# Kernel optimization log

Hardware: AMD Instinct MI355X
Metric: run time of the kernel (lower is better)

The kernel has to match this reference:

```python
import jax, jax.numpy as jnp
import numpy as np

B, N, D, H, MLP = 8, 1024, 1024, 16, 4096
DEPTH = D // H
EPS = 1e-6
INV_SQRT_DEPTH = 1.0 / np.sqrt(DEPTH).astype(np.float32)


def _linear_params(key, fan_in, fan_out):
    w = jax.random.normal(key, (fan_in, fan_out), dtype=jnp.float32) * 0.02
    b = jnp.zeros((fan_out,), dtype=jnp.float32)
    return w, b


def setup_inputs() -> dict:
    key = jax.random.key(0)
    ks = jax.random.split(key, 20)
    inp = {}
    inp['inputs'] = jax.random.normal(ks[0], (B, N, D), dtype=jnp.float32)
    inp['z'] = jax.random.normal(ks[1], (B, D), dtype=jnp.float32)
    # norm1 conditioning MLPs
    inp['n1_hw'], inp['n1_hb'] = _linear_params(ks[2], D, D)
    inp['n1_gw'], inp['n1_gb'] = _linear_params(ks[3], D, D)
    inp['n1_bw'], inp['n1_bb'] = _linear_params(ks[4], D, D)
    # attention
    inp['wq_w'], inp['wq_b'] = _linear_params(ks[5], D, D)
    inp['wk_w'], inp['wk_b'] = _linear_params(ks[6], D, D)
    inp['wv_w'], inp['wv_b'] = _linear_params(ks[7], D, D)
    inp['qa_w'], inp['qa_b'] = _linear_params(ks[8], D, H)
    inp['out_w'], inp['out_b'] = _linear_params(ks[9], D, D)
    # norm2 conditioning MLPs
    inp['n2_hw'], inp['n2_hb'] = _linear_params(ks[10], D, D)
    inp['n2_gw'], inp['n2_gb'] = _linear_params(ks[11], D, D)
    inp['n2_bw'], inp['n2_bb'] = _linear_params(ks[12], D, D)
    # MLP
    inp['mlp_w1'], inp['mlp_b1'] = _linear_params(ks[13], D, MLP)
    inp['mlp_w2'], inp['mlp_b2'] = _linear_params(ks[14], MLP, D)
    return inp


def _sm_norm(x, z, hw, hb, gw, gb, bw, bb):
    # LayerNorm over last dim, no affine
    mean = jnp.mean(x, axis=-1, keepdims=True)
    var = jnp.mean(jnp.square(x - mean), axis=-1, keepdims=True)
    xn = (x - mean) / jnp.sqrt(var + EPS)
    h = jax.nn.relu(z @ hw + hb)                 # [B, D]
    scale = (h @ gw + gb)[:, :, None]            # [B, D, 1]
    shift = (h @ bw + bb)[:, :, None]            # [B, D, 1]
    # broadcasts since N == D (as in the torch module)
    return xn * scale + shift


def _additive_attn(x, wq_w, wq_b, wk_w, wk_b, wv_w, wv_b, qa_w, qa_b, out_w, out_b):
    q = x @ wq_w + wq_b                          # [B, N, D]
    k = x @ wk_w + wk_b
    v = x @ wv_w + wv_b
    attn = jnp.transpose(q @ qa_w + qa_b, (0, 2, 1)) * INV_SQRT_DEPTH  # [B, H, N]
    attn = jax.nn.softmax(attn, axis=-1)
    qh = q.reshape(B, N, H, DEPTH).transpose(0, 2, 1, 3)  # [B, H, N, d]
    kh = k.reshape(B, N, H, DEPTH).transpose(0, 2, 1, 3)
    vh = v.reshape(B, N, H, DEPTH).transpose(0, 2, 1, 3)
    global_q = jnp.einsum('bhn,bhnd->bhd', attn, qh)[:, :, None, :]  # [B, H, 1, d]
    r = global_q * kh * vh                       # [B, H, N, d]
    r = r.transpose(0, 2, 1, 3).reshape(B, N, D)
    return r @ out_w + out_b, attn


def reference(inputs, z,
              n1_hw, n1_hb, n1_gw, n1_gb, n1_bw, n1_bb,
              wq_w, wq_b, wk_w, wk_b, wv_w, wv_b, qa_w, qa_b, out_w, out_b,
              n2_hw, n2_hb, n2_gw, n2_gb, n2_bw, n2_bb,
              mlp_w1, mlp_b1, mlp_w2, mlp_b2):
    x_norm1 = _sm_norm(inputs, z, n1_hw, n1_hb, n1_gw, n1_gb, n1_bw, n1_bb)
    attn_out, attn_maps = _additive_attn(x_norm1, wq_w, wq_b, wk_w, wk_b,
                                         wv_w, wv_b, qa_w, qa_b, out_w, out_b)
    attn_out = inputs + attn_out                 # dropout rate 0 -> identity
    x_norm2 = _sm_norm(attn_out, z, n2_hw, n2_hb, n2_gw, n2_gb, n2_bw, n2_bb)
    h = jax.nn.gelu(x_norm2 @ mlp_w1 + mlp_b1, approximate=False)
    mlp_out = h @ mlp_w2 + mlp_b2
    output = attn_out + mlp_out
    return output, attn_maps
```

## Files before the change

### kernel.cpp

```cpp
#include <hip/hip_runtime.h>
#include <math.h>


typedef __attribute__((ext_vector_type(8))) short short8;
typedef __attribute__((ext_vector_type(4))) float f32x4;

#define DEVI __device__ __forceinline__

DEVI unsigned short f2bf(float f) {
  union { float f; unsigned int u; } c; c.f = f;
  unsigned int r = c.u + 0x7fffu + ((c.u >> 16) & 1u);
  return (unsigned short)(r >> 16);
}
DEVI float bf2f(unsigned short u) {
  union { unsigned int u; float f; } c; c.u = ((unsigned int)u) << 16;
  return c.f;
}

DEVI void async16(const void* g, void* l) {
  __builtin_amdgcn_global_load_lds((const __attribute__((address_space(1))) void*)g,
                                   (__attribute__((address_space(3))) void*)l, 16, 0, 0);
}

__global__ void transpose_bf16_k(const float* __restrict__ in,
                                 unsigned short* __restrict__ out, int R, int C) {
  __shared__ float tile[32][33];
  const int c0 = blockIdx.x * 32, r0 = blockIdx.y * 32;
  const int tx = threadIdx.x, ty = threadIdx.y;
#pragma unroll
  for (int j = 0; j < 4; j++) {
    int r = r0 + ty + j * 8, c = c0 + tx;
    if (r < R && c < C) tile[ty + j * 8][tx] = in[(size_t)r * C + c];
  }
  __syncthreads();
#pragma unroll
  for (int j = 0; j < 4; j++) {
    int c = c0 + ty + j * 8, r = r0 + tx;
    if (c < C && r < R) out[(size_t)c * R + r] = f2bf(tile[tx][ty + j * 8]);
  }
}

__global__ void pad_bias_k(const float* __restrict__ qa_b, float* __restrict__ pad) {
  int t = threadIdx.x;
  pad[t] = (t < 16) ? qa_b[t] : 0.f;
}

__global__ void bias3_k(const float* __restrict__ b0, const float* __restrict__ b1,
                        const float* __restrict__ b2, float* __restrict__ out) {
  const int t = blockIdx.x * 256 + threadIdx.x;
  out[t] = (t < 1024) ? b0[t] : (t < 2048 ? b1[t - 1024] : b2[t - 2048]);
}

__global__ void zero_k(float4* __restrict__ p) {
  p[blockIdx.x * 256 + threadIdx.x] = float4{0.f, 0.f, 0.f, 0.f};
}

template <int NMAT>
__global__ __launch_bounds__(256) void skinny_k(const float* __restrict__ X,
                                                const float* __restrict__ W0,
                                                const float* __restrict__ W1,
                                                float* __restrict__ acc0,
                                                float* __restrict__ acc1) {
  const int tid = threadIdx.x;
  const int jt = blockIdx.x, kc = blockIdx.y;
  const int jl = tid & 63, kg = tid >> 6;
  const int jcol = jt * 64 + jl;
  __shared__ float xs[8][64];
  for (int i = tid; i < 512; i += 256) {
    const int b = i >> 6, kk = i & 63;
    xs[b][kk] = X[b * 1024 + kc * 64 + kk];
  }
  __syncthreads();
  float a0[8], a1[8];
#pragma unroll
  for (int b = 0; b < 8; b++) { a0[b] = 0.f; a1[b] = 0.f; }
#pragma unroll
  for (int kk = 0; kk < 16; kk++) {
    const int k = kg * 16 + kk;
    const float w0 = W0[(size_t)(kc * 64 + k) * 1024 + jcol];
#pragma unroll
    for (int b = 0; b < 8; b++) a0[b] += xs[b][k] * w0;
    if (NMAT == 2) {
      const float w1 = W1[(size_t)(kc * 64 + k) * 1024 + jcol];
#pragma unroll
      for (int b = 0; b < 8; b++) a1[b] += xs[b][k] * w1;
    }
  }
  __shared__ float red[256][9];
#pragma unroll
  for (int b = 0; b < 8; b++) red[tid][b] = a0[b];
  __syncthreads();
  if (tid < 64) {
#pragma unroll
    for (int b = 0; b < 8; b++) {
      const float s = red[tid][b] + red[tid + 64][b] + red[tid + 128][b] + red[tid + 192][b];
      atomicAdd(&acc0[b * 1024 + jcol], s);
    }
  }
  if (NMAT == 2) {
    __syncthreads();
#pragma unroll
    for (int b = 0; b < 8; b++) red[tid][b] = a1[b];
    __syncthreads();
    if (tid < 64) {
#pragma unroll
      for (int b = 0; b < 8; b++) {
        const float s = red[tid][b] + red[tid + 64][b] + red[tid + 128][b] + red[tid + 192][b];
        atomicAdd(&acc1[b * 1024 + jcol], s);
      }
    }
  }
}

__global__ void h_epi_k(const float* __restrict__ acc, const float* __restrict__ hb,
                        float* __restrict__ h) {
  const int i = blockIdx.x * 256 + threadIdx.x;
  h[i] = fmaxf(acc[i] + hb[i & 1023], 0.f);
}

__global__ __launch_bounds__(256) void ln_mod_k(const float* __restrict__ x,
                                                const float* __restrict__ s_acc,
                                                const float* __restrict__ t_acc,
                                                const float* __restrict__ gb,
                                                const float* __restrict__ bb,
                                                unsigned short* __restrict__ out) {
  const int lane = threadIdx.x & 63, wid = threadIdx.x >> 6;
  const size_t row = (size_t)blockIdx.x * 4 + wid;
  const int n = (int)(row & 1023);
  const float4* xr = (const float4*)(x + row * 1024);
  float4 v[4];
  float s = 0.f, ss = 0.f;
#pragma unroll
  for (int j = 0; j < 4; j++) {
    v[j] = xr[j * 64 + lane];
    s += v[j].x + v[j].y + v[j].z + v[j].w;
    ss += v[j].x * v[j].x + v[j].y * v[j].y + v[j].z * v[j].z + v[j].w * v[j].w;
  }
#pragma unroll
  for (int o = 32; o > 0; o >>= 1) { s += __shfl_xor(s, o); ss += __shfl_xor(ss, o); }
  const float mean = s * (1.f / 1024.f);
  const float var = ss * (1.f / 1024.f) - mean * mean;
  const float inv = rsqrtf(var + 1e-6f);
  const float scale = s_acc[row] + gb[n];
  const float shift = t_acc[row] + bb[n];
  const float sc = scale * inv;
  const float sh = shift - mean * sc;
#pragma unroll
  for (int j = 0; j < 4; j++) {
    ushort4 o4;
    o4.x = f2bf(v[j].x * sc + sh);
    o4.y = f2bf(v[j].y * sc + sh);
    o4.z = f2bf(v[j].z * sc + sh);
    o4.w = f2bf(v[j].w * sc + sh);
    *(ushort4*)(out + row * 1024 + (size_t)(j * 64 + lane) * 4) = o4;
  }
}

template <int EPI, int BM>
__global__ __launch_bounds__(512, 2) void gemm256(const unsigned short* __restrict__ A,
                                                  const unsigned short* __restrict__ BT,
                                                  const float* __restrict__ bias,
                                                  const float* __restrict__ resid,
                                                  void* __restrict__ Cout,
                                                  int M, int N, int K) {
  constexpr bool SWAP = (EPI == 0 || EPI == 1);
  constexpr int WROWS = BM / 2;
  constexpr int MF = WROWS / 16;
  constexpr int ALOADS = (BM * 8) / 512;
  constexpr int NLOADS = ALOADS + 4;
  __shared__ unsigned short lds[2 * BM * 64 + 2 * 256 * 64];
  unsigned short* As0 = lds;
  unsigned short* Bs0 = lds + 2 * BM * 64;
  const int tid = threadIdx.x;
  const int lane = tid & 63, w = tid >> 6;
  const int wm = w >> 2, wn = w & 3;
  const int lr = lane & 15;
  const int g0 = lane >> 4;
  const int nwg = gridDim.x * gridDim.y;
  const int rb = blockIdx.y * gridDim.x + blockIdx.x;
  const int sb = (rb & 7) * (nwg >> 3) + (rb >> 3);
  const size_t brow = (size_t)(sb / gridDim.x) * BM;
  const size_t bcol = (size_t)(sb % gridDim.x) * 256;
  const unsigned short* Ab = A + brow * (size_t)K;
  const unsigned short* Bb = BT + bcol * (size_t)K;
  const int NT = K >> 6;

  const f32x4 zero = {0.f, 0.f, 0.f, 0.f};
  f32x4 acc[MF][4];
#pragma unroll
  for (int m = 0; m < MF; m++)
#pragma unroll
    for (int n = 0; n < 4; n++) acc[m][n] = zero;

  auto stage = [&](int k0, int d) {
#pragma unroll
    for (int i = 0; i < ALOADS; i++) {
      const int c = i * 512 + tid;
      const int r = c >> 3, g = c & 7;
      const int gl = g ^ (r & 7);
      async16(Ab + (size_t)r * K + (k0 + gl * 8), &As0[(size_t)d * BM * 64 + c * 8]);
    }
#pragma unroll
    for (int i = 0; i < 4; i++) {
      const int c = i * 512 + tid;
      const int r = c >> 3, g = c & 7;
      const int gl = g ^ (r & 7);
      async16(Bb + (size_t)r * K + (k0 + gl * 8), &Bs0[(size_t)d * 256 * 64 + c * 8]);
    }
  };

  stage(0, 0);
  stage(64, 1);
  if constexpr (NLOADS == 8) asm volatile("s_waitcnt vmcnt(8)" ::: "memory");
  else asm volatile("s_waitcnt vmcnt(6)" ::: "memory");
  __builtin_amdgcn_s_barrier();

  for (int t = 0; t < NT; ++t) {
    const unsigned short* as = As0 + (size_t)(t & 1) * BM * 64;
    const unsigned short* bs = Bs0 + (size_t)(t & 1) * 256 * 64;
#pragma unroll
    for (int kk = 0; kk < 64; kk += 32) {
      const int gk = (kk >> 3) + g0;
      short8 bfrag[4];
#pragma unroll
      for (int nf = 0; nf < 4; nf++) {
        const int r = wn * 64 + nf * 16 + lr;
        bfrag[nf] = *(const short8*)&bs[r * 64 + ((gk ^ (r & 7)) << 3)];
      }
      __builtin_amdgcn_s_setprio(1);
#pragma unroll
      for (int mf = 0; mf < MF; mf++) {
        const int r = wm * WROWS + mf * 16 + lr;
        const short8 afrag = *(const short8*)&as[r * 64 + ((gk ^ (r & 7)) << 3)];
#pragma unroll
        for (int nf = 0; nf < 4; nf++) {
          if constexpr (SWAP)
            acc[mf][nf] = __builtin_amdgcn_mfma_f32_16x16x32_bf16(bfrag[nf], afrag, acc[mf][nf], 0, 0, 0);
          else
            acc[mf][nf] = __builtin_amdgcn_mfma_f32_16x16x32_bf16(afrag, bfrag[nf], acc[mf][nf], 0, 0, 0);
        }
      }
      __builtin_amdgcn_s_setprio(0);
    }
    asm volatile("" ::: "memory");
    __builtin_amdgcn_s_barrier();
    if (t + 2 < NT) {
      stage((t + 2) << 6, t & 1);
      if constexpr (NLOADS == 8) asm volatile("s_waitcnt vmcnt(8)" ::: "memory");
      else asm volatile("s_waitcnt vmcnt(6)" ::: "memory");
    } else {
      asm volatile("s_waitcnt vmcnt(0)" ::: "memory");
    }
    __builtin_amdgcn_s_barrier();
  }

  if constexpr (SWAP) {
    unsigned short* cst = lds;
    const int g4 = (lane >> 4) * 4;
#pragma unroll
    for (int nf = 0; nf < 4; nf++) {
#pragma unroll
      for (int mf = 0; mf < MF; mf++) {
        const int row = wm * WROWS + mf * 16 + lr;
        const int colb = wn * 64 + nf * 16 + g4;
        const float4 bv = *(const float4*)&bias[bcol + colb];
        float v[4];
#pragma unroll
        for (int j = 0; j < 4; j++) {
          v[j] = acc[mf][nf][j] + (&bv.x)[j];
          if (EPI == 1) v[j] = 0.5f * v[j] * (1.0f + erff(v[j] * 0.70710678118654752f));
        }
        ushort4 p;
        p.x = f2bf(v[0]); p.y = f2bf(v[1]); p.z = f2bf(v[2]); p.w = f2bf(v[3]);
        const int byo = row * 512 + ((colb * 2) ^ ((row & 7) << 4));
        *(ushort4*)((char*)cst + byo) = p;
      }
    }
    __syncthreads();
    unsigned short* outp;
    size_t ostride;
    if (EPI == 0) {
      outp = (unsigned short*)Cout + (size_t)(bcol >> 10) * ((size_t)M << 10) + (bcol & 1023);
      ostride = 1024;
    } else {
      outp = (unsigned short*)Cout + bcol;
      ostride = (size_t)N;
    }
#pragma unroll
    for (int it = 0; it < BM / 16; it++) {
      const int fl = it * 4096 + tid * 8;
      const int row = fl >> 8, colu = fl & 255;
      const int byo = row * 512 + ((colu * 2) ^ ((row & 7) << 4));
      const short8 val = *(const short8*)((char*)cst + byo);
      *(short8*)(outp + (size_t)(brow + row) * ostride + colu) = val;
    }
  } else {
    const int lc = lane & 15, lrow = (lane >> 4) * 4;
#pragma unroll
    for (int nf = 0; nf < 4; nf++) {
      const size_t col = bcol + wn * 64 + nf * 16 + lc;
      const float bv = bias[col];
#pragma unroll
      for (int mf = 0; mf < MF; mf++) {
#pragma unroll
        for (int j = 0; j < 4; j++) {
          const size_t row = brow + wm * WROWS + mf * 16 + lrow + j;
          const size_t idx = row * (size_t)N + col;
          ((float*)Cout)[idx] = acc[mf][nf][j] + bv + resid[idx];
        }
      }
    }
  }
}

template <int EPI>
__global__ __launch_bounds__(256) void gemm_bf16(const unsigned short* __restrict__ A,
                                                 const unsigned short* __restrict__ BT,
                                                 const float* __restrict__ bias,
                                                 const float* __restrict__ resid,
                                                 void* __restrict__ Cout,
                                                 int M, int N, int K) {
  __shared__ unsigned short As[128 * 64];
  __shared__ unsigned short Bs[128 * 64];
  const int tid = threadIdx.x;
  const int lane = tid & 63, wid = tid >> 6;
  const int wr = wid >> 1, wc = wid & 1;
  const size_t brow = (size_t)blockIdx.y * 128;
  const size_t bcol = (size_t)blockIdx.x * 128;
  const unsigned short* Ab = A + brow * (size_t)K;
  const unsigned short* Bb = BT + bcol * (size_t)K;

  const f32x4 zero = {0.f, 0.f, 0.f, 0.f};
  f32x4 acc[4][4];
#pragma unroll
  for (int m = 0; m < 4; m++)
#pragma unroll
    for (int n = 0; n < 4; n++) acc[m][n] = zero;

  for (int k0 = 0; k0 < K; k0 += 64) {
#pragma unroll
    for (int i = 0; i < 4; i++) {
      const int eo = (i * 256 + tid) * 8;
      const int r = eo >> 6, c = eo & 63;
      async16(Ab + (size_t)r * K + (k0 + c), &As[eo]);
      async16(Bb + (size_t)r * K + (k0 + c), &Bs[eo]);
    }
    __syncthreads();
    const int lr = lane & 15, lk = (lane >> 4) * 8;
#pragma unroll
    for (int kk = 0; kk < 64; kk += 32) {
      short8 af[4], bfv[4];
#pragma unroll
      for (int m = 0; m < 4; m++)
        af[m] = *(const short8*)&As[(wr * 64 + m * 16 + lr) * 64 + kk + lk];
#pragma unroll
      for (int n = 0; n < 4; n++)
        bfv[n] = *(const short8*)&Bs[(wc * 64 + n * 16 + lr) * 64 + kk + lk];
#pragma unroll
      for (int m = 0; m < 4; m++)
#pragma unroll
        for (int n = 0; n < 4; n++)
          acc[m][n] = __builtin_amdgcn_mfma_f32_16x16x32_bf16(af[m], bfv[n], acc[m][n], 0, 0, 0);
    }
    __syncthreads();
  }

  const int lc = lane & 15, lr4 = (lane >> 4) * 4;
#pragma unroll
  for (int n = 0; n < 4; n++) {
    const size_t col = bcol + wc * 64 + n * 16 + lc;
    const float bv = bias[col];
#pragma unroll
    for (int m = 0; m < 4; m++) {
#pragma unroll
      for (int j = 0; j < 4; j++) {
        const size_t row = brow + wr * 64 + m * 16 + lr4 + j;
        const size_t idx = row * (size_t)N + col;
        ((float*)Cout)[idx] = acc[m][n][j] + bv;
      }
    }
  }
}

__global__ __launch_bounds__(256) void softmax_k(const float* __restrict__ logits,
                                                 float* __restrict__ attn) {
  const int tid = threadIdx.x;
  const int bh = blockIdx.x;
  const int b = bh >> 4, h = bh & 15;
  __shared__ float redm[4];
  __shared__ float reds[4];
  float vals[4];
#pragma unroll
  for (int j = 0; j < 4; j++) {
    const int n = j * 256 + tid;
    vals[j] = logits[((size_t)b * 1024 + n) * 128 + h] * 0.125f;
  }
  float m = fmaxf(fmaxf(vals[0], vals[1]), fmaxf(vals[2], vals[3]));
#pragma unroll
  for (int o = 32; o > 0; o >>= 1) m = fmaxf(m, __shfl_xor(m, o));
  if ((tid & 63) == 0) redm[tid >> 6] = m;
  __syncthreads();
  m = fmaxf(fmaxf(redm[0], redm[1]), fmaxf(redm[2], redm[3]));
  float e[4];
  float s = 0.f;
#pragma unroll
  for (int j = 0; j < 4; j++) { e[j] = expf(vals[j] - m); s += e[j]; }
#pragma unroll
  for (int o = 32; o > 0; o >>= 1) s += __shfl_xor(s, o);
  if ((tid & 63) == 0) reds[tid >> 6] = s;
  __syncthreads();
  s = reds[0] + reds[1] + reds[2] + reds[3];
  const float invs = 1.f / s;
#pragma unroll
  for (int j = 0; j < 4; j++)
    attn[(size_t)bh * 1024 + j * 256 + tid] = e[j] * invs;
}

__global__ __launch_bounds__(256) void global_q_k(const float* __restrict__ attn,
                                                  const unsigned short* __restrict__ Q,
                                                  float* __restrict__ gq) {
  const int tid = threadIdx.x;
  const int bh = blockIdx.x;
  const int b = bh >> 4, h = bh & 15;
  const int d = tid & 63, g = tid >> 6;
  const float* arow = attn + (size_t)bh * 1024;
  const unsigned short* qcol = Q + (size_t)b * 1024 * 1024 + h * 64 + d;
  float acc = 0.f;
  for (int n = g * 256; n < g * 256 + 256; n++)
    acc += arow[n] * bf2f(qcol[(size_t)n * 1024]);
  __shared__ float red[256];
  red[tid] = acc;
  __syncthreads();
  if (g == 0) gq[(size_t)bh * 64 + d] = red[d] + red[64 + d] + red[128 + d] + red[192 + d];
}

__global__ __launch_bounds__(256) void r_k(const unsigned short* __restrict__ Kb,
                                           const unsigned short* __restrict__ Vb,
                                           const float* __restrict__ gq,
                                           unsigned short* __restrict__ R) {
  const size_t i = ((size_t)blockIdx.x * 256 + threadIdx.x) * 8;
  const int col = (int)(i & 1023);
  const size_t b = i >> 20;
  const int h = col >> 6, dd = col & 63;
  const float* g = gq + ((b << 4) + h) * 64 + dd;
  short8 kv = *(const short8*)(Kb + i);
  short8 vv = *(const short8*)(Vb + i);
  short8 r;
#pragma unroll
  for (int j = 0; j < 8; j++) {
    float f = g[j] * bf2f((unsigned short)kv[j]) * bf2f((unsigned short)vv[j]);
    r[j] = (short)f2bf(f);
  }
  *(short8*)(R + i) = r;
}

extern "C" void kernel_launch(void* const* d_in, const int* in_sizes, int n_in,
                              void* d_out, int out_size, void* d_ws, size_t ws_size,
                              hipStream_t stream) {
  (void)in_sizes; (void)n_in; (void)out_size; (void)ws_size;
  const float* inputs = (const float*)d_in[0];
  const float* z      = (const float*)d_in[1];
  const float* n1_hw = (const float*)d_in[2];  const float* n1_hb = (const float*)d_in[3];
  const float* n1_gw = (const float*)d_in[4];  const float* n1_gb = (const float*)d_in[5];
  const float* n1_bw = (const float*)d_in[6];  const float* n1_bb = (const float*)d_in[7];
  const float* wq_w  = (const float*)d_in[8];  const float* wq_b  = (const float*)d_in[9];
  const float* wk_w  = (const float*)d_in[10]; const float* wk_b  = (const float*)d_in[11];
  const float* wv_w  = (const float*)d_in[12]; const float* wv_b  = (const float*)d_in[13];
  const float* qa_w  = (const float*)d_in[14]; const float* qa_b  = (const float*)d_in[15];
  const float* out_w = (const float*)d_in[16]; const float* out_b = (const float*)d_in[17];
  const float* n2_hw = (const float*)d_in[18]; const float* n2_hb = (const float*)d_in[19];
  const float* n2_gw = (const float*)d_in[20]; const float* n2_gb = (const float*)d_in[21];
  const float* n2_bw = (const float*)d_in[22]; const float* n2_bb = (const float*)d_in[23];
  const float* mlp_w1 = (const float*)d_in[24]; const float* mlp_b1 = (const float*)d_in[25];
  const float* mlp_w2 = (const float*)d_in[26]; const float* mlp_b2 = (const float*)d_in[27];

  const int M = 8192, D = 1024, MLPD = 4096;

  char* ws = (char*)d_ws;
  size_t o = 0;
  auto alloc = [&](size_t bytes) -> char* {
    char* p = ws + o;
    o += (bytes + 255) & ~(size_t)255;
    return p;
  };
  unsigned short* wqkvT = (unsigned short*)alloc((size_t)3 * D * D * 2);
  unsigned short* woT = (unsigned short*)alloc((size_t)D * D * 2);
  unsigned short* w1T = (unsigned short*)alloc((size_t)MLPD * D * 2);
  unsigned short* w2T = (unsigned short*)alloc((size_t)D * MLPD * 2);
  unsigned short* qaT = (unsigned short*)alloc((size_t)128 * D * 2);
  unsigned short* xn  = (unsigned short*)alloc((size_t)M * D * 2);
  char* big = alloc((size_t)M * MLPD * 2);
  unsigned short* Qb = (unsigned short*)big;
  unsigned short* Kb = (unsigned short*)(big + (size_t)M * D * 2);
  unsigned short* Vb = (unsigned short*)(big + (size_t)M * D * 4);
  float* logits      = (float*)(big + (size_t)M * D * 6);
  unsigned short* hbuf = (unsigned short*)big;
  float* cacc  = (float*)alloc(6 * 8192 * 4);
  float* accH1 = cacc;
  float* accS1 = cacc + 1 * 8192;
  float* accT1 = cacc + 2 * 8192;
  float* accH2 = cacc + 3 * 8192;
  float* accS2 = cacc + 4 * 8192;
  float* accT2 = cacc + 5 * 8192;
  float* h1     = (float*)alloc(8 * 1024 * 4);
  float* h2     = (float*)alloc(8 * 1024 * 4);
  float* gq     = (float*)alloc(8 * 16 * 64 * 4);
  float* qa_b_pad = (float*)alloc(128 * 4);
  float* qkvb    = (float*)alloc(3072 * 4);

  float* out0 = (float*)d_out;
  float* attn = (float*)d_out + (size_t)M * D;

  const dim3 tb(32, 8);
  hipLaunchKernelGGL(transpose_bf16_k, dim3(32, 32), tb, 0, stream, wq_w, wqkvT, D, D);
  hipLaunchKernelGGL(transpose_bf16_k, dim3(32, 32), tb, 0, stream, wk_w, wqkvT + (size_t)D * D, D, D);
  hipLaunchKernelGGL(transpose_bf16_k, dim3(32, 32), tb, 0, stream, wv_w, wqkvT + (size_t)2 * D * D, D, D);
  hipLaunchKernelGGL(transpose_bf16_k, dim3(32, 32), tb, 0, stream, out_w, woT, D, D);
  hipLaunchKernelGGL(transpose_bf16_k, dim3(128, 32), tb, 0, stream, mlp_w1, w1T, D, MLPD);
  hipLaunchKernelGGL(transpose_bf16_k, dim3(32, 128), tb, 0, stream, mlp_w2, w2T, MLPD, D);
  hipLaunchKernelGGL(transpose_bf16_k, dim3(1, 32), tb, 0, stream, qa_w, qaT, D, 16);
  hipLaunchKernelGGL(pad_bias_k, dim3(1), dim3(128), 0, stream, qa_b, qa_b_pad);
  hipLaunchKernelGGL(bias3_k, dim3(12), dim3(256), 0, stream, wq_b, wk_b, wv_b, qkvb);

  hipLaunchKernelGGL(zero_k, dim3(48), dim3(256), 0, stream, (float4*)cacc);
  hipLaunchKernelGGL(skinny_k<1>, dim3(16, 16), dim3(256), 0, stream, z, n1_hw, (const float*)nullptr, accH1, (float*)nullptr);
  hipLaunchKernelGGL(h_epi_k, dim3(32), dim3(256), 0, stream, accH1, n1_hb, h1);
  hipLaunchKernelGGL(skinny_k<2>, dim3(16, 16), dim3(256), 0, stream, h1, n1_gw, n1_bw, accS1, accT1);
  hipLaunchKernelGGL(skinny_k<1>, dim3(16, 16), dim3(256), 0, stream, z, n2_hw, (const float*)nullptr, accH2, (float*)nullptr);
  hipLaunchKernelGGL(h_epi_k, dim3(32), dim3(256), 0, stream, accH2, n2_hb, h2);
  hipLaunchKernelGGL(skinny_k<2>, dim3(16, 16), dim3(256), 0, stream, h2, n2_gw, n2_bw, accS2, accT2);

  hipLaunchKernelGGL(ln_mod_k, dim3(M / 4), dim3(256), 0, stream, inputs, accS1, accT1, n1_gb, n1_bb, xn);

  hipLaunchKernelGGL((gemm256<0, 256>), dim3(12, 32), dim3(512), 0, stream, xn, wqkvT, qkvb, (const float*)nullptr, (void*)Qb, M, 3072, D);

  hipLaunchKernelGGL(gemm_bf16<3>, dim3(1, 64), dim3(256), 0, stream, Qb, qaT, qa_b_pad, (const float*)nullptr, (void*)logits, M, 128, D);

  hipLaunchKernelGGL(softmax_k, dim3(128), dim3(256), 0, stream, logits, attn);

  hipLaunchKernelGGL(global_q_k, dim3(128), dim3(256), 0, stream, attn, Qb, gq);

  hipLaunchKernelGGL(r_k, dim3(M * D / 8 / 256), dim3(256), 0, stream, Kb, Vb, gq, Kb);

  hipLaunchKernelGGL((gemm256<2, 128>), dim3(4, 64), dim3(512), 0, stream, Kb, woT, out_b, inputs, (void*)out0, M, D, D);

  hipLaunchKernelGGL(ln_mod_k, dim3(M / 4), dim3(256), 0, stream, out0, accS2, accT2, n2_gb, n2_bb, xn);

  hipLaunchKernelGGL((gemm256<1, 256>), dim3(16, 32), dim3(512), 0, stream, xn, w1T, mlp_b1, (const float*)nullptr, (void*)hbuf, M, MLPD, D);

  hipLaunchKernelGGL((gemm256<2, 128>), dim3(4, 64), dim3(512), 0, stream, hbuf, w2T, mlp_b2, out0, (void*)out0, M, D, MLPD);
}
```

Baseline: 667.7 us.

## Split GEMM K-tile into four phases interleaving async loads with MFMA sub-blocks

The bf16 GEMM main loop now divides each 64-wide K tile into four phases, each covering one quarter of the accumulator tile. Each phase issues one quarter of the next tile's global-to-LDS async loads, so memory traffic is spread across the compute instead of being issued in one burst after a barrier. The grouped block-index swizzle is replaced with a direct blockIdx mapping. The trade-off is a barrier after every phase instead of two per tile, and possibly worse L2 reuse now that the swizzle is gone.

Measured after the change: 647.4 us. 1.03x faster.

```diff
diff --git a/kernel.cpp b/kernel.cpp
--- a/kernel.cpp
+++ b/kernel.cpp
@@ -166,8 +166,8 @@
   constexpr bool SWAP = (EPI == 0 || EPI == 1);
   constexpr int WROWS = BM / 2;
   constexpr int MF = WROWS / 16;
-  constexpr int ALOADS = (BM * 8) / 512;
-  constexpr int NLOADS = ALOADS + 4;
+  constexpr int MPH = MF / 2;
+  constexpr int ALOADS_H = (WROWS * 64) / (512 * 8);
   __shared__ unsigned short lds[2 * BM * 64 + 2 * 256 * 64];
   unsigned short* As0 = lds;
   unsigned short* Bs0 = lds + 2 * BM * 64;
@@ -176,11 +176,8 @@
   const int wm = w >> 2, wn = w & 3;
   const int lr = lane & 15;
   const int g0 = lane >> 4;
-  const int nwg = gridDim.x * gridDim.y;
-  const int rb = blockIdx.y * gridDim.x + blockIdx.x;
-  const int sb = (rb & 7) * (nwg >> 3) + (rb >> 3);
-  const size_t brow = (size_t)(sb / gridDim.x) * BM;
-  const size_t bcol = (size_t)(sb % gridDim.x) * 256;
+  const size_t brow = (size_t)blockIdx.y * BM;
+  const size_t bcol = (size_t)blockIdx.x * 256;
   const unsigned short* Ab = A + brow * (size_t)K;
   const unsigned short* Bb = BT + bcol * (size_t)K;
   const int NT = K >> 6;
@@ -192,66 +189,85 @@
 #pragma unroll
     for (int n = 0; n < 4; n++) acc[m][n] = zero;
 
-  auto stage = [&](int k0, int d) {
-#pragma unroll
-    for (int i = 0; i < ALOADS; i++) {
+  auto stageA = [&](int t, int h) {
+    const int d = t & 1, k0 = t << 6;
+#pragma unroll
+    for (int i = 0; i < ALOADS_H; i++) {
       const int c = i * 512 + tid;
-      const int r = c >> 3, g = c & 7;
+      const int r = h * WROWS + (c >> 3), g = c & 7;
       const int gl = g ^ (r & 7);
-      async16(Ab + (size_t)r * K + (k0 + gl * 8), &As0[(size_t)d * BM * 64 + c * 8]);
-    }
-#pragma unroll
-    for (int i = 0; i < 4; i++) {
+      async16(Ab + (size_t)r * K + (k0 + gl * 8),
+              &As0[(size_t)d * BM * 64 + (size_t)h * WROWS * 64 + c * 8]);
+    }
+  };
+  auto stageB = [&](int t, int h) {
+    const int d = t & 1, k0 = t << 6;
+#pragma unroll
+    for (int i = 0; i < 2; i++) {
       const int c = i * 512 + tid;
-      const int r = c >> 3, g = c & 7;
+      const int r = h * 128 + (c >> 3), g = c & 7;
       const int gl = g ^ (r & 7);
-      async16(Bb + (size_t)r * K + (k0 + gl * 8), &Bs0[(size_t)d * 256 * 64 + c * 8]);
+      async16(Bb + (size_t)r * K + (k0 + gl * 8),
+              &Bs0[(size_t)d * 256 * 64 + (size_t)h * 128 * 64 + c * 8]);
     }
   };
 
-  stage(0, 0);
-  stage(64, 1);
-  if constexpr (NLOADS == 8) asm volatile("s_waitcnt vmcnt(8)" ::: "memory");
-  else asm volatile("s_waitcnt vmcnt(6)" ::: "memory");
-  __builtin_amdgcn_s_barrier();
+  stageA(0, 0); stageA(0, 1); stageB(0, 0); stageB(0, 1);
 
   for (int t = 0; t < NT; ++t) {
     const unsigned short* as = As0 + (size_t)(t & 1) * BM * 64;
     const unsigned short* bs = Bs0 + (size_t)(t & 1) * 256 * 64;
 #pragma unroll
-    for (int kk = 0; kk < 64; kk += 32) {
-      const int gk = (kk >> 3) + g0;
-      short8 bfrag[4];
-#pragma unroll
-      for (int nf = 0; nf < 4; nf++) {
-        const int r = wn * 64 + nf * 16 + lr;
-        bfrag[nf] = *(const short8*)&bs[r * 64 + ((gk ^ (r & 7)) << 3)];
+    for (int p = 0; p < 4; ++p) {
+      if (t + 1 < NT) {
+        if (p == 0) stageA(t + 1, 0);
+        else if (p == 1) stageA(t + 1, 1);
+        else if (p == 2) stageB(t + 1, 0);
+        else stageB(t + 1, 1);
+      }
+      if (p == 0) {
+        if (t + 1 < NT) {
+          if constexpr (ALOADS_H == 2) asm volatile("s_waitcnt vmcnt(2)" ::: "memory");
+          else asm volatile("s_waitcnt vmcnt(1)" ::: "memory");
+        } else {
+          asm volatile("s_waitcnt vmcnt(0)" ::: "memory");
+        }
+        __builtin_amdgcn_s_barrier();
+      }
+      const int mf0 = (p >> 1) * MPH;
+      const int nf0 = (p & 1) * 2;
+      short8 bfrag[2][2], afrag[2][MPH];
+#pragma unroll
+      for (int kki = 0; kki < 2; kki++) {
+        const int gk = kki * 4 + g0;
+#pragma unroll
+        for (int nf = 0; nf < 2; nf++) {
+          const int r = wn * 64 + (nf0 + nf) * 16 + lr;
+          bfrag[kki][nf] = *(const short8*)&bs[r * 64 + ((gk ^ (r & 7)) << 3)];
+        }
+#pragma unroll
+        for (int mf = 0; mf < MPH; mf++) {
+          const int r = wm * WROWS + (mf0 + mf) * 16 + lr;
+          afrag[kki][mf] = *(const short8*)&as[r * 64 + ((gk ^ (r & 7)) << 3)];
+        }
       }
       __builtin_amdgcn_s_setprio(1);
 #pragma unroll
-      for (int mf = 0; mf < MF; mf++) {
-        const int r = wm * WROWS + mf * 16 + lr;
-        const short8 afrag = *(const short8*)&as[r * 64 + ((gk ^ (r & 7)) << 3)];
-#pragma unroll
-        for (int nf = 0; nf < 4; nf++) {
-          if constexpr (SWAP)
-            acc[mf][nf] = __builtin_amdgcn_mfma_f32_16x16x32_bf16(bfrag[nf], afrag, acc[mf][nf], 0, 0, 0);
-          else
-            acc[mf][nf] = __builtin_amdgcn_mfma_f32_16x16x32_bf16(afrag, bfrag[nf], acc[mf][nf], 0, 0, 0);
-        }
-      }
+      for (int kki = 0; kki < 2; kki++)
+#pragma unroll
+        for (int mf = 0; mf < MPH; mf++)
+#pragma unroll
+          for (int nf = 0; nf < 2; nf++) {
+            if constexpr (SWAP)
+              acc[mf0 + mf][nf0 + nf] = __builtin_amdgcn_mfma_f32_16x16x32_bf16(
+                  bfrag[kki][nf], afrag[kki][mf], acc[mf0 + mf][nf0 + nf], 0, 0, 0);
+            else
+              acc[mf0 + mf][nf0 + nf] = __builtin_amdgcn_mfma_f32_16x16x32_bf16(
+                  afrag[kki][mf], bfrag[kki][nf], acc[mf0 + mf][nf0 + nf], 0, 0, 0);
+          }
       __builtin_amdgcn_s_setprio(0);
-    }
-    asm volatile("" ::: "memory");
-    __builtin_amdgcn_s_barrier();
-    if (t + 2 < NT) {
-      stage((t + 2) << 6, t & 1);
-      if constexpr (NLOADS == 8) asm volatile("s_waitcnt vmcnt(8)" ::: "memory");
-      else asm volatile("s_waitcnt vmcnt(6)" ::: "memory");
-    } else {
-      asm volatile("s_waitcnt vmcnt(0)" ::: "memory");
-    }
-    __builtin_amdgcn_s_barrier();
+      __builtin_amdgcn_s_barrier();
+    }
   }
 
   if constexpr (SWAP) {
@@ -270,10 +286,10 @@
           v[j] = acc[mf][nf][j] + (&bv.x)[j];
           if (EPI == 1) v[j] = 0.5f * v[j] * (1.0f + erff(v[j] * 0.70710678118654752f));
         }
-        ushort4 p;
-        p.x = f2bf(v[0]); p.y = f2bf(v[1]); p.z = f2bf(v[2]); p.w = f2bf(v[3]);
+        ushort4 pck;
+        pck.x = f2bf(v[0]); pck.y = f2bf(v[1]); pck.z = f2bf(v[2]); pck.w = f2bf(v[3]);
         const int byo = row * 512 + ((colb * 2) ^ ((row & 7) << 4));
-        *(ushort4*)((char*)cst + byo) = p;
+        *(ushort4*)((char*)cst + byo) = pck;
       }
     }
     __syncthreads();
```
